# Kernel tuning notes

Measured on AMD Instinct MI355X. Metric: run time of the kernel, lower is better.

The kernel has to match this reference:

```python
import jax, jax.numpy as jnp
import numpy as np

N_FEATS = 256
N_HEAD = 8
EPS_LN = 1e-5  # nn.LayerNorm default eps (both per-head K/V norms and final LN)


def sine_pos_embed(h, w, num_pos_feats, dtype=jnp.float32):
    """DETR PositionEmbeddingSine with normalize=True, mask=None -> [h, w, 2*num_pos_feats]."""
    eps = 1e-6
    scale = 2.0 * np.pi
    temperature = 10000.0
    # cumsum of ones == arange(1, n+1); normalized by last value (= h or w) + eps
    y = (jnp.arange(1, h + 1, dtype=dtype) / (h + eps) * scale)[:, None, None]  # [h,1,1]
    x = (jnp.arange(1, w + 1, dtype=dtype) / (w + eps) * scale)[None, :, None]  # [1,w,1]
    dim_t = jnp.arange(num_pos_feats, dtype=dtype)
    dim_t = temperature ** (2.0 * jnp.floor(dim_t / 2.0) / num_pos_feats)

    def interleave(t):
        # stack(sin(t[0::2]), cos(t[1::2])).flatten -> sin,cos interleaved
        return jnp.stack((jnp.sin(t[..., 0::2]), jnp.cos(t[..., 1::2])), axis=-1).reshape(
            t.shape[:-1] + (num_pos_feats,))

    py = jnp.broadcast_to(interleave(y / dim_t), (h, w, num_pos_feats))
    px = jnp.broadcast_to(interleave(x / dim_t), (h, w, num_pos_feats))
    return jnp.concatenate((py, px), axis=-1)  # channel order: [pos_y, pos_x]


def _ln(t, g, b, eps=EPS_LN):
    mu = jnp.mean(t, axis=-1, keepdims=True)
    var = jnp.var(t, axis=-1, keepdims=True)
    return (t - mu) * jax.lax.rsqrt(var + eps) * g + b


def setup_inputs() -> dict:
    key = jax.random.key(0)
    ks = jax.random.split(key, 4)
    b, c, h, w = 8, N_FEATS, 128, 128
    d_k = c // N_HEAD
    s = 0.02
    return dict(
        x=jax.random.normal(ks[0], (b, c, h, w), jnp.float32),
        Wq=jax.random.normal(ks[1], (c, c), jnp.float32) * s,
        bq=jnp.zeros((c,), jnp.float32),
        Wk=jax.random.normal(ks[2], (c, c), jnp.float32) * s,
        bk=jnp.zeros((c,), jnp.float32),
        Wv=jax.random.normal(ks[3], (c, c), jnp.float32) * s,
        bv=jnp.zeros((c,), jnp.float32),
        gK=jnp.ones((N_HEAD, d_k), jnp.float32),
        bK=jnp.zeros((N_HEAD, d_k), jnp.float32),
        gV=jnp.ones((N_HEAD, d_k), jnp.float32),
        bV=jnp.zeros((N_HEAD, d_k), jnp.float32),
        g_ln=jnp.ones((c,), jnp.float32),
        b_ln=jnp.zeros((c,), jnp.float32),
    )


def reference(x, Wq, bq, Wk, bk, Wv, bv, gK, bK, gV, bV, g_ln, b_ln):
    b, c, h, w = x.shape
    d_k = c // N_HEAD
    n = h * w
    pos = sine_pos_embed(h, w, c // 2, dtype=x.dtype).reshape(1, n, c)
    xs = jnp.transpose(x, (0, 2, 3, 1)).reshape(b, n, c)  # [b, n, c]
    qk_in = xs + pos

    def proj(t, W, bias):
        # torch Linear: t @ W.T + b, then split heads -> [b, H, n, d_k]
        return (t @ W.T + bias).reshape(b, n, N_HEAD, d_k).transpose(0, 2, 1, 3)

    q = proj(qk_in, Wq, bq)
    k = proj(qk_in, Wk, bk)
    v = proj(xs, Wv, bv)

    # galerkin: per-head LayerNorm over d_k on K and V (learnable per-head affine)
    k = _ln(k, gK[None, :, None, :], bK[None, :, None, :])
    v = _ln(v, gV[None, :, None, :], bV[None, :, None, :])

    # linear (galerkin) attention: Q @ (K^T V) / seq_len  (attn dropout p=0.0)
    scores = jnp.einsum('bhnd,bhne->bhde', k, v) / n  # [b, H, d_k, d_k]
    out = jnp.einsum('bhnd,bhde->bhne', q, scores)    # [b, H, n, d_k]
    out = out.transpose(0, 2, 1, 3).reshape(b, n, c)

    out = out + out  # x = x + dropout(x); dropout identity at inference
    out = _ln(out, g_ln, b_ln)
    return jnp.transpose(out.reshape(b, h, w, c), (0, 3, 1, 2))  # [b, c, h, w]
```

## Files before the change

### kernel.cpp

```cpp
#include <hip/hip_runtime.h>


typedef float floatx4 __attribute__((ext_vector_type(4)));
typedef __bf16 bf16x8 __attribute__((ext_vector_type(8)));
typedef unsigned short ushortx8 __attribute__((ext_vector_type(8)));
typedef unsigned short ushort;

static __device__ __forceinline__ ushort f2bf(float f) {
  unsigned int u = __builtin_bit_cast(unsigned int, f);
  u += 0x7FFFu + ((u >> 16) & 1u);
  return (ushort)(u >> 16);
}
static __device__ __forceinline__ floatx4 mfma16(bf16x8 a, bf16x8 b, floatx4 c) {
  return __builtin_amdgcn_mfma_f32_16x16x32_bf16(a, b, c, 0, 0, 0);
}
static __device__ __forceinline__ bf16x8 frag(const ushort* p) {
  return *(const bf16x8*)p;
}
typedef __attribute__((address_space(3))) unsigned int as3_u32;
typedef __attribute__((address_space(1))) const unsigned int as1_u32;
static __device__ __forceinline__ void gl_lds16(const ushort* g, ushort* l) {
  __builtin_amdgcn_global_load_lds((as1_u32*)g, (as3_u32*)l, 16, 0, 0);
}

__global__ __launch_bounds__(256) void prep_w(const float* __restrict__ Wk,
                                              const float* __restrict__ Wv,
                                              ushort* __restrict__ Wkbf,
                                              ushort* __restrict__ Wvbf) {
  const int i = (int)blockIdx.x * 256 + (int)threadIdx.x;
  float4 a = ((const float4*)Wk)[i];
  float4 b = ((const float4*)Wv)[i];
  ushort4 ua = {f2bf(a.x), f2bf(a.y), f2bf(a.z), f2bf(a.w)};
  ushort4 ub = {f2bf(b.x), f2bf(b.y), f2bf(b.z), f2bf(b.w)};
  ((ushort4*)Wkbf)[i] = ua;
  ((ushort4*)Wvbf)[i] = ub;
}

__global__ __launch_bounds__(256) void prep_qx(const float* __restrict__ x,
                                               ushort* __restrict__ qkT,
                                               ushort* __restrict__ xT, int b0) {
  __shared__ float tile[64 * 68];
  const int t = (int)threadIdx.x;
  const int z = (int)blockIdx.y;
  const int b = b0 + z;
  const int n0 = (int)blockIdx.x * 64;
  const float* xb = x + (size_t)b * 256 * 16384;
  ushort* qb = qkT + (size_t)z * 16384 * 256;
  ushort* xtb = xT + (size_t)z * 16384 * 256;
  for (int kc = 0; kc < 4; ++kc) {
    if (kc) __syncthreads();
    const int nn = (t & 15) * 4;
    const int r0 = t >> 4;
#pragma unroll
    for (int it = 0; it < 4; ++it) {
      const int k = r0 + it * 16;
      const float4 v = *(const float4*)(xb + (size_t)(kc * 64 + k) * 16384 + n0 + nn);
      tile[(nn + 0) * 68 + k] = v.x;
      tile[(nn + 1) * 68 + k] = v.y;
      tile[(nn + 2) * 68 + k] = v.z;
      tile[(nn + 3) * 68 + k] = v.w;
    }
    __syncthreads();
#pragma unroll
    for (int it = 0; it < 2; ++it) {
      const int P = t + it * 256;
      const int r = P >> 3;
      const int p = P & 7;
      const int n = n0 + r;
      const int i = n >> 7, j = n & 127;
      ushortx8 uq, ux;
#pragma unroll
      for (int e = 0; e < 8; ++e) {
        const int kg = kc * 64 + p * 8 + e;
        const int kk = kg & 127;
        const float coord = ((kg < 128) ? (float)(i + 1) : (float)(j + 1)) *
                            (6.283185307179586f / (128.0f + 1e-6f));
        const float inv = exp2f(-13.287712379549449f * (float)(kk >> 1) * (1.0f / 64.0f));
        const float arg = coord * inv;
        const float pe = (kk & 1) ? __cosf(arg) : __sinf(arg);
        const float xv = tile[r * 68 + p * 8 + e];
        ux[e] = f2bf(xv);
        uq[e] = f2bf(xv + pe);
      }
      const int sw = (p ^ (r & 7)) * 8;
      *(ushortx8*)(qb + (size_t)n * 256 + kc * 64 + sw) = uq;
      *(ushortx8*)(xtb + (size_t)n * 256 + kc * 64 + sw) = ux;
    }
  }
}

#define LDC 72
#define NT 4
__global__ __launch_bounds__(256, 2) void kv_scores(
    const ushort* __restrict__ qkT, const ushort* __restrict__ xT,
    const ushort* __restrict__ Wkbf, const ushort* __restrict__ Wvbf,
    const float* __restrict__ bk, const float* __restrict__ bv,
    const float* __restrict__ gK, const float* __restrict__ bKp,
    const float* __restrict__ gV, const float* __restrict__ bVp,
    float* __restrict__ scores) {
  __shared__ ushort SQ[128 * 64];
  __shared__ ushort SX[128 * 64];
  __shared__ ushort KT[128 * LDC];
  __shared__ ushort VT[128 * LDC];
  const int t = (int)threadIdx.x, lane = t & 63, w = t >> 6;
  const int l15 = lane & 15, l4 = lane >> 4;
  const int hv = (int)blockIdx.y, z = (int)blockIdx.z;
  const ushort* qb = qkT + (size_t)z * 16384 * 256;
  const ushort* xb = xT + (size_t)z * 16384 * 256;
  const int ocb = hv * 128 + w * 32;
  const int h = hv * 4 + w;
  const float bkv[2] = {bk[ocb + l15], bk[ocb + 16 + l15]};
  const float bvv[2] = {bv[ocb + l15], bv[ocb + 16 + l15]};
  const float gk0 = gK[h * 32 + l15], gk1 = gK[h * 32 + 16 + l15];
  const float ok0 = bKp[h * 32 + l15], ok1 = bKp[h * 32 + 16 + l15];
  const float gv0 = gV[h * 32 + l15], gv1 = gV[h * 32 + 16 + l15];
  const float ov0 = bVp[h * 32 + l15], ov1 = bVp[h * 32 + 16 + l15];
  const int srow = w * 32 + (lane >> 3);
  const int scol = (lane & 7) * 8;
  const int rsw = l15 & 7;
  floatx4 sacc[2][2] = {};
  for (int nt = 0; nt < NT; ++nt) {
    const int n0 = ((int)blockIdx.x * NT + nt) * 128;
    floatx4 acck[2][8] = {};
    floatx4 accv[2][8] = {};
    for (int kc = 0; kc < 4; ++kc) {
      __syncthreads();
#pragma unroll
      for (int j = 0; j < 4; ++j) {
        const int r = srow + j * 8;
        const size_t go = (size_t)(n0 + r) * 256 + kc * 64 + scol;
        gl_lds16(qb + go, SQ + w * 2048 + j * 512);
        gl_lds16(xb + go, SX + w * 2048 + j * 512);
      }
      bf16x8 Bk[2][2], Bv[2][2];
#pragma unroll
      for (int ci = 0; ci < 2; ++ci) {
        const int kb = (kc * 2 + ci) * 32 + l4 * 8;
        Bk[ci][0] = frag(Wkbf + (ocb + l15) * 256 + kb);
        Bk[ci][1] = frag(Wkbf + (ocb + 16 + l15) * 256 + kb);
        Bv[ci][0] = frag(Wvbf + (ocb + l15) * 256 + kb);
        Bv[ci][1] = frag(Wvbf + (ocb + 16 + l15) * 256 + kb);
      }
      __syncthreads();
#pragma unroll
      for (int ci = 0; ci < 2; ++ci) {
#pragma unroll
        for (int m = 0; m < 8; ++m) {
          const int row = m * 16 + l15;
          const int off = row * 64 + ((ci * 4 + l4) ^ rsw) * 8;
          const bf16x8 aq = *(const bf16x8*)(SQ + off);
          const bf16x8 ax = *(const bf16x8*)(SX + off);
          acck[0][m] = mfma16(aq, Bk[ci][0], acck[0][m]);
          acck[1][m] = mfma16(aq, Bk[ci][1], acck[1][m]);
          accv[0][m] = mfma16(ax, Bv[ci][0], accv[0][m]);
          accv[1][m] = mfma16(ax, Bv[ci][1], accv[1][m]);
        }
      }
    }
#pragma unroll
    for (int tt = 0; tt < 2; ++tt)
#pragma unroll
      for (int m = 0; m < 8; ++m)
#pragma unroll
        for (int r = 0; r < 4; ++r) {
          acck[tt][m][r] += bkv[tt];
          accv[tt][m][r] += bvv[tt];
        }
#pragma unroll
    for (int m = 0; m < 8; ++m) {
#pragma unroll
      for (int r = 0; r < 4; ++r) {
        {
          const float a0 = acck[0][m][r], a1 = acck[1][m][r];
          float s = a0 + a1, q = a0 * a0 + a1 * a1;
#pragma unroll
          for (int msk = 1; msk < 16; msk <<= 1) {
            s += __shfl_xor(s, msk);
            q += __shfl_xor(q, msk);
          }
          const float mu = s * (1.0f / 32.0f);
          const float rstd = rsqrtf(q * (1.0f / 32.0f) - mu * mu + 1e-5f);
          acck[0][m][r] = (a0 - mu) * rstd * gk0 + ok0;
          acck[1][m][r] = (a1 - mu) * rstd * gk1 + ok1;
        }
        {
          const float a0 = accv[0][m][r], a1 = accv[1][m][r];
          float s = a0 + a1, q = a0 * a0 + a1 * a1;
#pragma unroll
          for (int msk = 1; msk < 16; msk <<= 1) {
            s += __shfl_xor(s, msk);
            q += __shfl_xor(q, msk);
          }
          const float mu = s * (1.0f / 32.0f);
          const float rstd = rsqrtf(q * (1.0f / 32.0f) - mu * mu + 1e-5f);
          accv[0][m][r] = (a0 - mu) * rstd * gv0 + ov0;
          accv[1][m][r] = (a1 - mu) * rstd * gv1 + ov1;
        }
      }
    }
#pragma unroll
    for (int half = 0; half < 2; ++half) {
      __syncthreads();
#pragma unroll
      for (int tt = 0; tt < 2; ++tt) {
        const int ch = w * 32 + tt * 16 + l15;
#pragma unroll
        for (int mm = 0; mm < 4; ++mm) {
          const int m = half * 4 + mm;
          const int col = mm * 16 + l4 * 4;
          ushort4 uk = {f2bf(acck[tt][m][0]), f2bf(acck[tt][m][1]),
                        f2bf(acck[tt][m][2]), f2bf(acck[tt][m][3])};
          ushort4 uv = {f2bf(accv[tt][m][0]), f2bf(accv[tt][m][1]),
                        f2bf(accv[tt][m][2]), f2bf(accv[tt][m][3])};
          *(ushort4*)(KT + ch * LDC + col) = uk;
          *(ushort4*)(VT + ch * LDC + col) = uv;
        }
      }
      __syncthreads();
#pragma unroll
      for (int nk = 0; nk < 2; ++nk) {
        const int ko = nk * 32 + l4 * 8;
        const bf16x8 ka0 = *(const bf16x8*)(KT + (w * 32 + l15) * LDC + ko);
        const bf16x8 ka1 = *(const bf16x8*)(KT + (w * 32 + 16 + l15) * LDC + ko);
        const bf16x8 vb0 = *(const bf16x8*)(VT + (w * 32 + l15) * LDC + ko);
        const bf16x8 vb1 = *(const bf16x8*)(VT + (w * 32 + 16 + l15) * LDC + ko);
        sacc[0][0] = mfma16(ka0, vb0, sacc[0][0]);
        sacc[0][1] = mfma16(ka0, vb1, sacc[0][1]);
        sacc[1][0] = mfma16(ka1, vb0, sacc[1][0]);
        sacc[1][1] = mfma16(ka1, vb1, sacc[1][1]);
      }
    }
  }
#pragma unroll
  for (int di = 0; di < 2; ++di)
#pragma unroll
    for (int ej = 0; ej < 2; ++ej)
#pragma unroll
      for (int r = 0; r < 4; ++r) {
        const int d = di * 16 + l4 * 4 + r;
        const int e = ej * 16 + l15;
        atomicAdd(scores + ((size_t)(z * 8 + h) * 32 + d) * 32 + e, sacc[di][ej][r]);
      }
}

__global__ __launch_bounds__(256) void w2_kernel(
    const float* __restrict__ Wq, const float* __restrict__ bq,
    const float* __restrict__ scores, ushort* __restrict__ W2bf,
    float* __restrict__ b2) {
  const int z = (int)blockIdx.y;
  const int row = (int)blockIdx.x;
  const int t = (int)threadIdx.x;
  const float inv_n = 1.0f / 16384.0f;
  const float* sc = scores + (size_t)z * 8192;
  if (row < 256) {
    const int h = row >> 5, e = row & 31;
    float s = 0.0f;
#pragma unroll
    for (int d = 0; d < 32; ++d)
      s += Wq[(h * 32 + d) * 256 + t] * sc[(h * 32 + d) * 32 + e];
    W2bf[(size_t)z * 65536 + row * 256 + t] = f2bf(s * inv_n);
  } else {
    const int h = t >> 5, e = t & 31;
    float s = 0.0f;
#pragma unroll
    for (int d = 0; d < 32; ++d)
      s += bq[h * 32 + d] * sc[(h * 32 + d) * 32 + e];
    b2[z * 256 + t] = s * inv_n;
  }
}

__global__ __launch_bounds__(256, 2) void out_kernel(
    const ushort* __restrict__ qkT, const ushort* __restrict__ W2bf,
    const float* __restrict__ b2, const float* __restrict__ g_ln,
    const float* __restrict__ b_ln, float* __restrict__ out, int b0) {
  const int t = (int)threadIdx.x, lane = t & 63, w = t >> 6;
  const int l15 = lane & 15, l4 = lane >> 4;
  const int z = (int)blockIdx.y, b = b0 + z;
  const int n0 = (int)blockIdx.x * 64;
  const ushort* qb = qkT + (size_t)z * 16384 * 256;
  const ushort* W2b = W2bf + (size_t)z * 65536;
  const int row = n0 + w * 16 + l15;
  const int rsw = l15 & 7;
  floatx4 acc[16] = {};
#pragma unroll
  for (int c = 0; c < 8; ++c) {
    const int kb = c * 32 + l4 * 8;
    const int off = (c >> 1) * 64 + ((((c & 1) * 4 + l4) ^ rsw)) * 8;
    const bf16x8 a = frag(qb + (size_t)row * 256 + off);
#pragma unroll
    for (int tt = 0; tt < 16; ++tt) {
      const bf16x8 bb = frag(W2b + (tt * 16 + l15) * 256 + kb);
      acc[tt] = mfma16(a, bb, acc[tt]);
    }
  }
#pragma unroll
  for (int tt = 0; tt < 16; ++tt) {
    const float b2v = b2[z * 256 + tt * 16 + l15];
#pragma unroll
    for (int r = 0; r < 4; ++r) acc[tt][r] = 2.0f * (acc[tt][r] + b2v);
  }
  float mean[4], rstd[4];
#pragma unroll
  for (int r = 0; r < 4; ++r) {
    float s = 0.0f, q = 0.0f;
#pragma unroll
    for (int tt = 0; tt < 16; ++tt) {
      const float v = acc[tt][r];
      s += v;
      q += v * v;
    }
#pragma unroll
    for (int msk = 1; msk < 16; msk <<= 1) {
      s += __shfl_xor(s, msk);
      q += __shfl_xor(q, msk);
    }
    const float mu = s * (1.0f / 256.0f);
    mean[r] = mu;
    rstd[r] = rsqrtf(q * (1.0f / 256.0f) - mu * mu + 1e-5f);
  }
#pragma unroll
  for (int tt = 0; tt < 16; ++tt) {
    const int c = tt * 16 + l15;
    const float g = g_ln[c], be = b_ln[c];
    float4 o;
    o.x = (acc[tt][0] - mean[0]) * rstd[0] * g + be;
    o.y = (acc[tt][1] - mean[1]) * rstd[1] * g + be;
    o.z = (acc[tt][2] - mean[2]) * rstd[2] * g + be;
    o.w = (acc[tt][3] - mean[3]) * rstd[3] * g + be;
    *(float4*)(out + (size_t)(b * 256 + c) * 16384 + n0 + w * 16 + l4 * 4) = o;
  }
}

extern "C" void kernel_launch(void* const* d_in, const int* in_sizes, int n_in,
                              void* d_out, int out_size, void* d_ws, size_t ws_size,
                              hipStream_t stream) {
  (void)in_sizes; (void)n_in; (void)out_size;
  const float* x   = (const float*)d_in[0];
  const float* Wq  = (const float*)d_in[1];
  const float* bq  = (const float*)d_in[2];
  const float* Wk  = (const float*)d_in[3];
  const float* bk  = (const float*)d_in[4];
  const float* Wv  = (const float*)d_in[5];
  const float* bv  = (const float*)d_in[6];
  const float* gK  = (const float*)d_in[7];
  const float* bK  = (const float*)d_in[8];
  const float* gV  = (const float*)d_in[9];
  const float* bV  = (const float*)d_in[10];
  const float* gln = (const float*)d_in[11];
  const float* bln = (const float*)d_in[12];
  float* out = (float*)d_out;

  const size_t PB = 16384ULL * 256 * 2;
  const size_t W2SZ = 131072, SCSZ = 32768, B2SZ = 1024, WKV = 262144;
  int g = 8;
  while (g > 1 && ws_size < (size_t)g * (2 * PB + W2SZ + SCSZ + B2SZ) + WKV) g >>= 1;

  char* p = (char*)d_ws;
  ushort* qkT   = (ushort*)p; p += (size_t)g * PB;
  ushort* xT    = (ushort*)p; p += (size_t)g * PB;
  ushort* Wkbf  = (ushort*)p; p += 131072;
  ushort* Wvbf  = (ushort*)p; p += 131072;
  ushort* W2bf  = (ushort*)p; p += (size_t)g * W2SZ;
  float*  scores = (float*)p; p += (size_t)g * SCSZ;
  float*  b2    = (float*)p;

  prep_w<<<dim3(64), 256, 0, stream>>>(Wk, Wv, Wkbf, Wvbf);
  for (int b0 = 0; b0 < 8; b0 += g) {
    hipMemsetAsync(scores, 0, (size_t)g * SCSZ, stream);
    prep_qx<<<dim3(256, g), 256, 0, stream>>>(x, qkT, xT, b0);
    kv_scores<<<dim3(128 / NT, 2, g), 256, 0, stream>>>(qkT, xT, Wkbf, Wvbf, bk, bv,
                                                        gK, bK, gV, bV, scores);
    w2_kernel<<<dim3(257, g), 256, 0, stream>>>(Wq, bq, scores, W2bf, b2);
    out_kernel<<<dim3(256, g), 256, 0, stream>>>(qkT, W2bf, b2, gln, bln, out, b0);
  }
}
```

Before: 560.1 us.

## Fold positional embedding into projection via separable row/column bias tables

Result: slower. 632.7 us (+13.0%).

```diff
diff --git a/kernel.cpp b/kernel.cpp
--- a/kernel.cpp
+++ b/kernel.cpp
@@ -36,8 +36,55 @@
   ((ushort4*)Wvbf)[i] = ub;
 }
 
+__global__ __launch_bounds__(256) void poswk(const float* __restrict__ Wk,
+                                             const float* __restrict__ bk,
+                                             float* __restrict__ PyKb,
+                                             float* __restrict__ PxKT) {
+  __shared__ float pe[128];
+  const int ii = (int)blockIdx.x, t = (int)threadIdx.x;
+  if (t < 128) {
+    const float coord = (float)(ii + 1) * (6.283185307179586f / (128.0f + 1e-6f));
+    const float inv = exp2f(-13.287712379549449f * (float)(t >> 1) * (1.0f / 64.0f));
+    const float arg = coord * inv;
+    pe[t] = (t & 1) ? cosf(arg) : sinf(arg);
+  }
+  __syncthreads();
+  const float* wrow = Wk + (size_t)t * 256;
+  float py = bk[t], px = 0.0f;
+#pragma unroll 8
+  for (int kk = 0; kk < 128; ++kk) {
+    py += pe[kk] * wrow[kk];
+    px += pe[kk] * wrow[128 + kk];
+  }
+  PyKb[ii * 256 + t] = py;
+  PxKT[t * 128 + ii] = px;
+}
+
+__global__ __launch_bounds__(256) void posw2(const float* __restrict__ W2f,
+                                             const float* __restrict__ b2,
+                                             float* __restrict__ Py2b,
+                                             float* __restrict__ Px2T) {
+  __shared__ float pe[128];
+  const int ii = (int)blockIdx.x, z = (int)blockIdx.y, t = (int)threadIdx.x;
+  if (t < 128) {
+    const float coord = (float)(ii + 1) * (6.283185307179586f / (128.0f + 1e-6f));
+    const float inv = exp2f(-13.287712379549449f * (float)(t >> 1) * (1.0f / 64.0f));
+    const float arg = coord * inv;
+    pe[t] = (t & 1) ? cosf(arg) : sinf(arg);
+  }
+  __syncthreads();
+  const float* wrow = W2f + (size_t)z * 65536 + (size_t)t * 256;
+  float py = b2[z * 256 + t], px = 0.0f;
+#pragma unroll 8
+  for (int kk = 0; kk < 128; ++kk) {
+    py += pe[kk] * wrow[kk];
+    px += pe[kk] * wrow[128 + kk];
+  }
+  Py2b[((size_t)z * 128 + ii) * 256 + t] = py;
+  Px2T[(size_t)z * 32768 + t * 128 + ii] = px;
+}
+
 __global__ __launch_bounds__(256) void prep_qx(const float* __restrict__ x,
-                                               ushort* __restrict__ qkT,
                                                ushort* __restrict__ xT, int b0) {
   __shared__ float tile[64 * 68];
   const int t = (int)threadIdx.x;
@@ -45,7 +92,6 @@
   const int b = b0 + z;
   const int n0 = (int)blockIdx.x * 64;
   const float* xb = x + (size_t)b * 256 * 16384;
-  ushort* qb = qkT + (size_t)z * 16384 * 256;
   ushort* xtb = xT + (size_t)z * 16384 * 256;
   for (int kc = 0; kc < 4; ++kc) {
     if (kc) __syncthreads();
@@ -67,50 +113,34 @@
       const int r = P >> 3;
       const int p = P & 7;
       const int n = n0 + r;
-      const int i = n >> 7, j = n & 127;
-      ushortx8 uq, ux;
-#pragma unroll
-      for (int e = 0; e < 8; ++e) {
-        const int kg = kc * 64 + p * 8 + e;
-        const int kk = kg & 127;
-        const float coord = ((kg < 128) ? (float)(i + 1) : (float)(j + 1)) *
-                            (6.283185307179586f / (128.0f + 1e-6f));
-        const float inv = exp2f(-13.287712379549449f * (float)(kk >> 1) * (1.0f / 64.0f));
-        const float arg = coord * inv;
-        const float pe = (kk & 1) ? __cosf(arg) : __sinf(arg);
-        const float xv = tile[r * 68 + p * 8 + e];
-        ux[e] = f2bf(xv);
-        uq[e] = f2bf(xv + pe);
-      }
+      ushortx8 ux;
+#pragma unroll
+      for (int e = 0; e < 8; ++e) ux[e] = f2bf(tile[r * 68 + p * 8 + e]);
       const int sw = (p ^ (r & 7)) * 8;
-      *(ushortx8*)(qb + (size_t)n * 256 + kc * 64 + sw) = uq;
       *(ushortx8*)(xtb + (size_t)n * 256 + kc * 64 + sw) = ux;
     }
   }
 }
 
-#define LDC 72
-#define NT 4
+#define LDC2 40
 __global__ __launch_bounds__(256, 2) void kv_scores(
-    const ushort* __restrict__ qkT, const ushort* __restrict__ xT,
-    const ushort* __restrict__ Wkbf, const ushort* __restrict__ Wvbf,
-    const float* __restrict__ bk, const float* __restrict__ bv,
+    const ushort* __restrict__ xT, const ushort* __restrict__ Wkbf,
+    const ushort* __restrict__ Wvbf, const float* __restrict__ bv,
     const float* __restrict__ gK, const float* __restrict__ bKp,
     const float* __restrict__ gV, const float* __restrict__ bVp,
+    const float* __restrict__ PyKb, const float* __restrict__ PxKT,
     float* __restrict__ scores) {
-  __shared__ ushort SQ[128 * 64];
-  __shared__ ushort SX[128 * 64];
-  __shared__ ushort KT[128 * LDC];
-  __shared__ ushort VT[128 * LDC];
+  __shared__ ushort SQ[2][128 * 64];
+  __shared__ ushort KT[128 * LDC2];
+  __shared__ ushort VT[128 * LDC2];
   const int t = (int)threadIdx.x, lane = t & 63, w = t >> 6;
   const int l15 = lane & 15, l4 = lane >> 4;
   const int hv = (int)blockIdx.y, z = (int)blockIdx.z;
-  const ushort* qb = qkT + (size_t)z * 16384 * 256;
+  const int bx = (int)blockIdx.x;
   const ushort* xb = xT + (size_t)z * 16384 * 256;
   const int ocb = hv * 128 + w * 32;
   const int h = hv * 4 + w;
-  const float bkv[2] = {bk[ocb + l15], bk[ocb + 16 + l15]};
-  const float bvv[2] = {bv[ocb + l15], bv[ocb + 16 + l15]};
+  const float bvv0 = bv[ocb + l15], bvv1 = bv[ocb + 16 + l15];
   const float gk0 = gK[h * 32 + l15], gk1 = gK[h * 32 + 16 + l15];
   const float ok0 = bKp[h * 32 + l15], ok1 = bKp[h * 32 + 16 + l15];
   const float gv0 = gV[h * 32 + l15], gv1 = gV[h * 32 + 16 + l15];
@@ -118,117 +148,133 @@
   const int srow = w * 32 + (lane >> 3);
   const int scol = (lane & 7) * 8;
   const int rsw = l15 & 7;
+
+  auto issue = [&](int s) {
+    const int n0s = (bx * 4 + (s >> 2)) * 128;
+    const int kcs = (s & 3) * 64;
+    ushort* dst = &SQ[s & 1][w * 2048];
+    const ushort* src = xb + (size_t)(n0s + srow) * 256 + kcs + scol;
+#pragma unroll
+    for (int j = 0; j < 4; ++j) gl_lds16(src + (size_t)j * 8 * 256, dst + j * 512);
+  };
+  issue(0);
+
   floatx4 sacc[2][2] = {};
-  for (int nt = 0; nt < NT; ++nt) {
-    const int n0 = ((int)blockIdx.x * NT + nt) * 128;
+  for (int nt = 0; nt < 4; ++nt) {
+    const int i_nt = bx * 4 + nt;
     floatx4 acck[2][8] = {};
     floatx4 accv[2][8] = {};
+    float py0 = 0.f, py1 = 0.f;
+    float4 pxq0[2][2];
     for (int kc = 0; kc < 4; ++kc) {
+      const int s = nt * 4 + kc;
       __syncthreads();
-#pragma unroll
-      for (int j = 0; j < 4; ++j) {
-        const int r = srow + j * 8;
-        const size_t go = (size_t)(n0 + r) * 256 + kc * 64 + scol;
-        gl_lds16(qb + go, SQ + w * 2048 + j * 512);
-        gl_lds16(xb + go, SX + w * 2048 + j * 512);
-      }
-      bf16x8 Bk[2][2], Bv[2][2];
+      bf16x8 Bk0[2], Bk1[2], Bv0[2], Bv1[2];
 #pragma unroll
       for (int ci = 0; ci < 2; ++ci) {
         const int kb = (kc * 2 + ci) * 32 + l4 * 8;
-        Bk[ci][0] = frag(Wkbf + (ocb + l15) * 256 + kb);
-        Bk[ci][1] = frag(Wkbf + (ocb + 16 + l15) * 256 + kb);
-        Bv[ci][0] = frag(Wvbf + (ocb + l15) * 256 + kb);
-        Bv[ci][1] = frag(Wvbf + (ocb + 16 + l15) * 256 + kb);
-      }
-      __syncthreads();
+        Bk0[ci] = frag(Wkbf + (ocb + l15) * 256 + kb);
+        Bk1[ci] = frag(Wkbf + (ocb + 16 + l15) * 256 + kb);
+        Bv0[ci] = frag(Wvbf + (ocb + l15) * 256 + kb);
+        Bv1[ci] = frag(Wvbf + (ocb + 16 + l15) * 256 + kb);
+      }
+      if (kc == 3) {
+        py0 = PyKb[i_nt * 256 + ocb + l15];
+        py1 = PyKb[i_nt * 256 + ocb + 16 + l15];
+#pragma unroll
+        for (int mm = 0; mm < 2; ++mm) {
+          pxq0[0][mm] = *(const float4*)(PxKT + (ocb + l15) * 128 + mm * 16 + l4 * 4);
+          pxq0[1][mm] = *(const float4*)(PxKT + (ocb + 16 + l15) * 128 + mm * 16 + l4 * 4);
+        }
+      }
+      if (s < 15) issue(s + 1);
+      const ushort* sq = &SQ[s & 1][0];
 #pragma unroll
       for (int ci = 0; ci < 2; ++ci) {
 #pragma unroll
         for (int m = 0; m < 8; ++m) {
-          const int row = m * 16 + l15;
-          const int off = row * 64 + ((ci * 4 + l4) ^ rsw) * 8;
-          const bf16x8 aq = *(const bf16x8*)(SQ + off);
-          const bf16x8 ax = *(const bf16x8*)(SX + off);
-          acck[0][m] = mfma16(aq, Bk[ci][0], acck[0][m]);
-          acck[1][m] = mfma16(aq, Bk[ci][1], acck[1][m]);
-          accv[0][m] = mfma16(ax, Bv[ci][0], accv[0][m]);
-          accv[1][m] = mfma16(ax, Bv[ci][1], accv[1][m]);
+          const int off = (m * 16 + l15) * 64 + ((ci * 4 + l4) ^ rsw) * 8;
+          const bf16x8 a = *(const bf16x8*)(sq + off);
+          acck[0][m] = mfma16(a, Bk0[ci], acck[0][m]);
+          acck[1][m] = mfma16(a, Bk1[ci], acck[1][m]);
+          accv[0][m] = mfma16(a, Bv0[ci], accv[0][m]);
+          accv[1][m] = mfma16(a, Bv1[ci], accv[1][m]);
         }
       }
     }
 #pragma unroll
-    for (int tt = 0; tt < 2; ++tt)
-#pragma unroll
-      for (int m = 0; m < 8; ++m)
+    for (int q = 0; q < 4; ++q) {
+#pragma unroll
+      for (int mm = 0; mm < 2; ++mm) {
+        const int m = q * 2 + mm;
+        float4 px0, px1;
+        if (q == 0) {
+          px0 = pxq0[0][mm];
+          px1 = pxq0[1][mm];
+        } else {
+          px0 = *(const float4*)(PxKT + (ocb + l15) * 128 + m * 16 + l4 * 4);
+          px1 = *(const float4*)(PxKT + (ocb + 16 + l15) * 128 + m * 16 + l4 * 4);
+        }
+        const float px0a[4] = {px0.x, px0.y, px0.z, px0.w};
+        const float px1a[4] = {px1.x, px1.y, px1.z, px1.w};
 #pragma unroll
         for (int r = 0; r < 4; ++r) {
-          acck[tt][m][r] += bkv[tt];
-          accv[tt][m][r] += bvv[tt];
+          {
+            const float a0 = acck[0][m][r] + py0 + px0a[r];
+            const float a1 = acck[1][m][r] + py1 + px1a[r];
+            float sum = a0 + a1, sq2 = a0 * a0 + a1 * a1;
+#pragma unroll
+            for (int msk = 1; msk < 16; msk <<= 1) {
+              sum += __shfl_xor(sum, msk);
+              sq2 += __shfl_xor(sq2, msk);
+            }
+            const float mu = sum * (1.0f / 32.0f);
+            const float rstd = rsqrtf(sq2 * (1.0f / 32.0f) - mu * mu + 1e-5f);
+            acck[0][m][r] = (a0 - mu) * rstd * gk0 + ok0;
+            acck[1][m][r] = (a1 - mu) * rstd * gk1 + ok1;
+          }
+          {
+            const float a0 = accv[0][m][r] + bvv0;
+            const float a1 = accv[1][m][r] + bvv1;
+            float sum = a0 + a1, sq2 = a0 * a0 + a1 * a1;
+#pragma unroll
+            for (int msk = 1; msk < 16; msk <<= 1) {
+              sum += __shfl_xor(sum, msk);
+              sq2 += __shfl_xor(sq2, msk);
+            }
+            const float mu = sum * (1.0f / 32.0f);
+            const float rstd = rsqrtf(sq2 * (1.0f / 32.0f) - mu * mu + 1e-5f);
+            accv[0][m][r] = (a0 - mu) * rstd * gv0 + ov0;
+            accv[1][m][r] = (a1 - mu) * rstd * gv1 + ov1;
+          }
         }
-#pragma unroll
-    for (int m = 0; m < 8; ++m) {
-#pragma unroll
-      for (int r = 0; r < 4; ++r) {
-        {
-          const float a0 = acck[0][m][r], a1 = acck[1][m][r];
-          float s = a0 + a1, q = a0 * a0 + a1 * a1;
-#pragma unroll
-          for (int msk = 1; msk < 16; msk <<= 1) {
-            s += __shfl_xor(s, msk);
-            q += __shfl_xor(q, msk);
-          }
-          const float mu = s * (1.0f / 32.0f);
-          const float rstd = rsqrtf(q * (1.0f / 32.0f) - mu * mu + 1e-5f);
-          acck[0][m][r] = (a0 - mu) * rstd * gk0 + ok0;
-          acck[1][m][r] = (a1 - mu) * rstd * gk1 + ok1;
-        }
-        {
-          const float a0 = accv[0][m][r], a1 = accv[1][m][r];
-          float s = a0 + a1, q = a0 * a0 + a1 * a1;
-#pragma unroll
-          for (int msk = 1; msk < 16; msk <<= 1) {
-            s += __shfl_xor(s, msk);
-            q += __shfl_xor(q, msk);
-          }
-          const float mu = s * (1.0f / 32.0f);
-          const float rstd = rsqrtf(q * (1.0f / 32.0f) - mu * mu + 1e-5f);
-          accv[0][m][r] = (a0 - mu) * rstd * gv0 + ov0;
-          accv[1][m][r] = (a1 - mu) * rstd * gv1 + ov1;
-        }
-      }
-    }
-#pragma unroll
-    for (int half = 0; half < 2; ++half) {
+      }
       __syncthreads();
 #pragma unroll
       for (int tt = 0; tt < 2; ++tt) {
         const int ch = w * 32 + tt * 16 + l15;
 #pragma unroll
-        for (int mm = 0; mm < 4; ++mm) {
-          const int m = half * 4 + mm;
+        for (int mm = 0; mm < 2; ++mm) {
+          const int m = q * 2 + mm;
           const int col = mm * 16 + l4 * 4;
           ushort4 uk = {f2bf(acck[tt][m][0]), f2bf(acck[tt][m][1]),
                         f2bf(acck[tt][m][2]), f2bf(acck[tt][m][3])};
           ushort4 uv = {f2bf(accv[tt][m][0]), f2bf(accv[tt][m][1]),
                         f2bf(accv[tt][m][2]), f2bf(accv[tt][m][3])};
-          *(ushort4*)(KT + ch * LDC + col) = uk;
-          *(ushort4*)(VT + ch * LDC + col) = uv;
+          *(ushort4*)(KT + ch * LDC2 + col) = uk;
+          *(ushort4*)(VT + ch * LDC2 + col) = uv;
         }
       }
       __syncthreads();
-#pragma unroll
-      for (int nk = 0; nk < 2; ++nk) {
-        const int ko = nk * 32 + l4 * 8;
-        const bf16x8 ka0 = *(const bf16x8*)(KT + (w * 32 + l15) * LDC + ko);
-        const bf16x8 ka1 = *(const bf16x8*)(KT + (w * 32 + 16 + l15) * LDC + ko);
-        const bf16x8 vb0 = *(const bf16x8*)(VT + (w * 32 + l15) * LDC + ko);
-        const bf16x8 vb1 = *(const bf16x8*)(VT + (w * 32 + 16 + l15) * LDC + ko);
-        sacc[0][0] = mfma16(ka0, vb0, sacc[0][0]);
-        sacc[0][1] = mfma16(ka0, vb1, sacc[0][1]);
-        sacc[1][0] = mfma16(ka1, vb0, sacc[1][0]);
-        sacc[1][1] = mfma16(ka1, vb1, sacc[1][1]);
-      }
+      const int ko = l4 * 8;
+      const bf16x8 ka0 = *(const bf16x8*)(KT + (w * 32 + l15) * LDC2 + ko);
+      const bf16x8 ka1 = *(const bf16x8*)(KT + (w * 32 + 16 + l15) * LDC2 + ko);
+      const bf16x8 vb0 = *(const bf16x8*)(VT + (w * 32 + l15) * LDC2 + ko);
+      const bf16x8 vb1 = *(const bf16x8*)(VT + (w * 32 + 16 + l15) * LDC2 + ko);
+      sacc[0][0] = mfma16(ka0, vb0, sacc[0][0]);
+      sacc[0][1] = mfma16(ka0, vb1, sacc[0][1]);
+      sacc[1][0] = mfma16(ka1, vb0, sacc[1][0]);
+      sacc[1][1] = mfma16(ka1, vb1, sacc[1][1]);
     }
   }
 #pragma unroll
@@ -246,7 +292,7 @@
 __global__ __launch_bounds__(256) void w2_kernel(
     const float* __restrict__ Wq, const float* __restrict__ bq,
     const float* __restrict__ scores, ushort* __restrict__ W2bf,
-    float* __restrict__ b2) {
+    float* __restrict__ W2f, float* __restrict__ b2) {
   const int z = (int)blockIdx.y;
   const int row = (int)blockIdx.x;
   const int t = (int)threadIdx.x;
@@ -258,7 +304,9 @@
 #pragma unroll
     for (int d = 0; d < 32; ++d)
       s += Wq[(h * 32 + d) * 256 + t] * sc[(h * 32 + d) * 32 + e];
-    W2bf[(size_t)z * 65536 + row * 256 + t] = f2bf(s * inv_n);
+    const float v = s * inv_n;
+    W2bf[(size_t)z * 65536 + row * 256 + t] = f2bf(v);
+    W2f[(size_t)z * 65536 + row * 256 + t] = v;
   } else {
     const int h = t >> 5, e = t & 31;
     float s = 0.0f;
@@ -270,15 +318,20 @@
 }
 
 __global__ __launch_bounds__(256, 2) void out_kernel(
-    const ushort* __restrict__ qkT, const ushort* __restrict__ W2bf,
-    const float* __restrict__ b2, const float* __restrict__ g_ln,
-    const float* __restrict__ b_ln, float* __restrict__ out, int b0) {
+    const ushort* __restrict__ xT, const ushort* __restrict__ W2bf,
+    const float* __restrict__ Py2b, const float* __restrict__ Px2T,
+    const float* __restrict__ g_ln, const float* __restrict__ b_ln,
+    float* __restrict__ out, int b0) {
   const int t = (int)threadIdx.x, lane = t & 63, w = t >> 6;
   const int l15 = lane & 15, l4 = lane >> 4;
   const int z = (int)blockIdx.y, b = b0 + z;
-  const int n0 = (int)blockIdx.x * 64;
-  const ushort* qb = qkT + (size_t)z * 16384 * 256;
+  const int bx = (int)blockIdx.x;
+  const int n0 = bx * 64;
+  const ushort* xb = xT + (size_t)z * 16384 * 256;
   const ushort* W2b = W2bf + (size_t)z * 65536;
+  const float* py = Py2b + ((size_t)z * 128 + (bx >> 1)) * 256;
+  const float* pxT = Px2T + (size_t)z * 32768;
+  const int jbase = (bx & 1) * 64 + w * 16 + l4 * 4;
   const int row = n0 + w * 16 + l15;
   const int rsw = l15 & 7;
   floatx4 acc[16] = {};
@@ -286,7 +339,7 @@
   for (int c = 0; c < 8; ++c) {
     const int kb = c * 32 + l4 * 8;
     const int off = (c >> 1) * 64 + ((((c & 1) * 4 + l4) ^ rsw)) * 8;
-    const bf16x8 a = frag(qb + (size_t)row * 256 + off);
+    const bf16x8 a = frag(xb + (size_t)row * 256 + off);
 #pragma unroll
     for (int tt = 0; tt < 16; ++tt) {
       const bf16x8 bb = frag(W2b + (tt * 16 + l15) * 256 + kb);
@@ -295,9 +348,12 @@
   }
 #pragma unroll
   for (int tt = 0; tt < 16; ++tt) {
-    const float b2v = b2[z * 256 + tt * 16 + l15];
-#pragma unroll
-    for (int r = 0; r < 4; ++r) acc[tt][r] = 2.0f * (acc[tt][r] + b2v);
+    const int c = tt * 16 + l15;
+    const float pyv = py[c];
+    const float4 px = *(const float4*)(pxT + c * 128 + jbase);
+    const float pxa[4] = {px.x, px.y, px.z, px.w};
+#pragma unroll
+    for (int r = 0; r < 4; ++r) acc[tt][r] = 2.0f * (acc[tt][r] + pyv + pxa[r]);
   }
   float mean[4], rstd[4];
 #pragma unroll
@@ -351,26 +407,34 @@
   float* out = (float*)d_out;
 
   const size_t PB = 16384ULL * 256 * 2;
-  const size_t W2SZ = 131072, SCSZ = 32768, B2SZ = 1024, WKV = 262144;
+  const size_t PERZ = PB + 131072 + 262144 + 32768 + 1024 + 131072 + 131072;
+  const size_t SHARED = 262144 + 262144;
   int g = 8;
-  while (g > 1 && ws_size < (size_t)g * (2 * PB + W2SZ + SCSZ + B2SZ) + WKV) g >>= 1;
+  while (g > 1 && ws_size < (size_t)g * PERZ + SHARED) g >>= 1;
 
   char* p = (char*)d_ws;
-  ushort* qkT   = (ushort*)p; p += (size_t)g * PB;
   ushort* xT    = (ushort*)p; p += (size_t)g * PB;
   ushort* Wkbf  = (ushort*)p; p += 131072;
   ushort* Wvbf  = (ushort*)p; p += 131072;
-  ushort* W2bf  = (ushort*)p; p += (size_t)g * W2SZ;
-  float*  scores = (float*)p; p += (size_t)g * SCSZ;
+  float*  PyKb  = (float*)p;  p += 131072;
+  float*  PxKT  = (float*)p;  p += 131072;
+  ushort* W2bf  = (ushort*)p; p += (size_t)g * 131072;
+  float*  W2f   = (float*)p;  p += (size_t)g * 262144;
+  float*  Py2b  = (float*)p;  p += (size_t)g * 131072;
+  float*  Px2T  = (float*)p;  p += (size_t)g * 131072;
+  float*  scores = (float*)p; p += (size_t)g * 32768;
   float*  b2    = (float*)p;
 
   prep_w<<<dim3(64), 256, 0, stream>>>(Wk, Wv, Wkbf, Wvbf);
+  poswk<<<dim3(128), 256, 0, stream>>>(Wk, bk, PyKb, PxKT);
   for (int b0 = 0; b0 < 8; b0 += g) {
-    hipMemsetAsync(scores, 0, (size_t)g * SCSZ, stream);
-    prep_qx<<<dim3(256, g), 256, 0, stream>>>(x, qkT, xT, b0);
-    kv_scores<<<dim3(128 / NT, 2, g), 256, 0, stream>>>(qkT, xT, Wkbf, Wvbf, bk, bv,
-                                                        gK, bK, gV, bV, scores);
-    w2_kernel<<<dim3(257, g), 256, 0, stream>>>(Wq, bq, scores, W2bf, b2);
-    out_kernel<<<dim3(256, g), 256, 0, stream>>>(qkT, W2bf, b2, gln, bln, out, b0);
-  }
-}
+    hipMemsetAsync(scores, 0, (size_t)g * 32768, stream);
+    prep_qx<<<dim3(256, g), 256, 0, stream>>>(x, xT, b0);
+    kv_scores<<<dim3(32, 2, g), 256, 0, stream>>>(xT, Wkbf, Wvbf, bv, gK, bK,
+                                                  gV, bV, PyKb, PxKT, scores);
+    w2_kernel<<<dim3(257, g), 256, 0, stream>>>(Wq, bq, scores, W2bf, W2f, b2);
+    posw2<<<dim3(128, g), 256, 0, stream>>>(W2f, b2, Py2b, Px2T);
+    out_kernel<<<dim3(256, g), 256, 0, stream>>>(xT, W2bf, Py2b, Px2T, gln, bln,
+                                                 out, b0);
+  }
+}
```
